# Performance work log

Hardware: AMD Instinct MI355X
Metric: run time of the kernel (lower is better)

Reference implementation:

```python
import jax, jax.numpy as jnp
import numpy as np

B, C, D, O = 262144, 256, 64, 8


def setup_inputs() -> dict:
    key = jax.random.key(0)
    k1, k2, k3, k4 = jax.random.split(key, 4)
    inputs = jax.random.normal(k1, (B, D), dtype=jnp.float32)
    cluster_centers = jax.random.normal(k2, (C, D), dtype=jnp.float32)
    # widths initialized ~ N(1.0, 0.05) as in the layer
    widths = 1.0 + 0.05 * jax.random.normal(k3, (C,), dtype=jnp.float32)
    # rule_weights ~ N(0, 0.05)
    rule_weights = 0.05 * jax.random.normal(k4, (C, O), dtype=jnp.float32)
    return {"inputs": inputs, "cluster_centers": cluster_centers,
            "widths": widths, "rule_weights": rule_weights}


def reference(inputs, cluster_centers, widths, rule_weights):
    # Squared L2 distances via ||a-c||^2 = ||a||^2 + ||c||^2 - 2 a.c
    # (avoids materializing the [B, C, D] broadcast diff tensor)
    x_sq = jnp.sum(inputs * inputs, axis=1, keepdims=True)          # [B, 1]
    c_sq = jnp.sum(cluster_centers * cluster_centers, axis=1)       # [C]
    cross = inputs @ cluster_centers.T                               # [B, C]
    dists_squared = x_sq + c_sq[None, :] - 2.0 * cross               # [B, C]
    # Gaussian membership with per-cluster widths
    memb = jnp.exp(-dists_squared / (2.0 * widths * widths))         # [B, C]
    # Normalize over clusters (sum-normalization, not softmax-of-logits)
    memb_norm = memb / jnp.sum(memb, axis=1, keepdims=True)          # [B, C]
    # Weighted rule consequents
    return memb_norm @ rule_weights                                  # [B, O]
```

## Files before the change

kernel.cpp:

```cpp
#include <hip/hip_runtime.h>


#define NB 262144
#define NC 256
#define ND 64
#define NO 8

typedef __attribute__((ext_vector_type(8))) short short8;
typedef __attribute__((ext_vector_type(16))) float floatx16;

__device__ __host__ inline unsigned short f2bf(float f) {
    unsigned u = __builtin_bit_cast(unsigned, f);
    u = u + 0x7FFFu + ((u >> 16) & 1u);
    return (unsigned short)(u >> 16);
}
__device__ inline float bf2f(unsigned short s) {
    unsigned u = ((unsigned)s) << 16;
    return __builtin_bit_cast(float, u);
}

__global__ void fuzzy_prep(const float* __restrict__ centers,
                           const float* __restrict__ widths,
                           const float* __restrict__ W,
                           unsigned short* __restrict__ ws) {
    const int lane = threadIdx.x;
    const int col = lane & 31;
    const int h = lane >> 5;

    if (blockIdx.x < 8) {
        const int t = blockIdx.x;
        const int c = 32 * t + ((col & 19) | ((col & 4) << 1) | ((col & 8) >> 1));
        const float* cr = centers + c * ND;
        float w = widths[c];
        float kk = 1.4426950408889634f / (2.0f * w * w);

        float vv[4][8];
        float part = 0.0f;
#pragma unroll
        for (int kd = 0; kd < 4; ++kd) {
            const float4* p = (const float4*)(cr + kd * 16 + h * 8);
            float4 a0 = p[0], a1 = p[1];
            vv[kd][0] = a0.x; vv[kd][1] = a0.y; vv[kd][2] = a0.z; vv[kd][3] = a0.w;
            vv[kd][4] = a1.x; vv[kd][5] = a1.y; vv[kd][6] = a1.z; vv[kd][7] = a1.w;
#pragma unroll
            for (int j = 0; j < 8; ++j) part = fmaf(vv[kd][j], vv[kd][j], part);
        }
        float csq = part + __shfl_xor(part, 32, 64);

        unsigned short* base = ws;
#pragma unroll
        for (int kd = 0; kd < 4; ++kd) {
#pragma unroll
            for (int j = 0; j < 8; ++j) {
                float a = 2.0f * kk * vv[kd][j];
                unsigned short ah = f2bf(a);
                unsigned short al = f2bf(a - bf2f(ah));
                base[((t * 9 + kd) * 64 + lane) * 8 + j] = ah;
                base[((t * 9 + 4 + kd) * 64 + lane) * 8 + j] = al;
            }
        }
        unsigned short v[8] = {0, 0, 0, 0, 0, 0, 0, 0};
        if (h == 0) {
            float Bc = csq * kk;
            float kl = kk - bf2f(f2bf(kk));
            float Bl = Bc - bf2f(f2bf(Bc));
            v[0] = f2bf(-kk);
            v[1] = f2bf(-kk);
            v[2] = f2bf(-kl);
            v[3] = f2bf(-Bc);
            v[4] = f2bf(-Bl);
        }
#pragma unroll
        for (int j = 0; j < 8; ++j)
            base[((t * 9 + 8) * 64 + lane) * 8 + j] = v[j];
    } else {
        unsigned short* wbase = ws + 8 * 9 * 64 * 8;
        const int k2base = (blockIdx.x - 8) * 4;
#pragma unroll
        for (int kq = 0; kq < 4; ++kq) {
            int k2 = k2base + kq;
#pragma unroll
            for (int j = 0; j < 8; ++j) {
                int c = k2 * 16 + h * 8 + j;
                float val = (col < NO) ? W[c * NO + col] : (col == 8 ? 1.0f : 0.0f);
                wbase[(k2 * 64 + lane) * 8 + j] = f2bf(val);
            }
        }
    }
}

__global__ __launch_bounds__(256) void fuzzy_main(const float* __restrict__ x,
                                                  const short8* __restrict__ afrag,
                                                  const short8* __restrict__ wfrag,
                                                  float* __restrict__ out) {
    const int tid = threadIdx.x;
    const int wave = tid >> 6;
    const int lane = tid & 63;
    const int col = lane & 31;
    const int h = lane >> 5;
    const int bbase = (blockIdx.x * 4 + wave) * 64;

    short8 xh[2][4], xl[2][4];
    short8 f12[2];
#pragma unroll
    for (int u = 0; u < 2; ++u) {
        const float* xrow = x + (size_t)(bbase + u * 32 + col) * ND;
        float part = 0.0f;
#pragma unroll
        for (int kd = 0; kd < 4; ++kd) {
            const float4* p = (const float4*)(xrow + kd * 16 + h * 8);
            float4 v0 = p[0], v1 = p[1];
            float v[8] = {v0.x, v0.y, v0.z, v0.w, v1.x, v1.y, v1.z, v1.w};
            short8 hi, lo;
#pragma unroll
            for (int j = 0; j < 8; ++j) {
                part = fmaf(v[j], v[j], part);
                unsigned short hb = f2bf(v[j]);
                hi[j] = (short)hb;
                lo[j] = (short)(__builtin_bit_cast(unsigned, v[j] - bf2f(hb)) >> 16);
            }
            xh[u][kd] = hi;
            xl[u][kd] = lo;
        }
        float xsq = part + __shfl_xor(part, 32, 64);
        unsigned short sh = f2bf(xsq);
        unsigned short sl = f2bf(xsq - bf2f(sh));
        short8 f;
#pragma unroll
        for (int j = 0; j < 8; ++j) f[j] = 0;
        if (h == 0) {
            f[0] = (short)sh;
            f[1] = (short)sl;
            f[2] = (short)sh;
            f[3] = (short)0x3F80;
            f[4] = (short)0x3F80;
        }
        f12[u] = f;
    }

    floatx16 acc2[2];
#pragma unroll
    for (int u = 0; u < 2; ++u)
#pragma unroll
        for (int i = 0; i < 16; ++i) acc2[u][i] = 0.0f;

    const short8* ap = afrag + lane;
    const short8* wp = wfrag + lane;

#pragma unroll 2
    for (int t = 0; t < 8; ++t) {
        short8 A0 = ap[(t * 9 + 0) * 64];
        short8 A1 = ap[(t * 9 + 1) * 64];
        short8 A2 = ap[(t * 9 + 2) * 64];
        short8 A3 = ap[(t * 9 + 3) * 64];
        short8 L0 = ap[(t * 9 + 4) * 64];
        short8 L1 = ap[(t * 9 + 5) * 64];
        short8 L2 = ap[(t * 9 + 6) * 64];
        short8 L3 = ap[(t * 9 + 7) * 64];
        short8 C12 = ap[(t * 9 + 8) * 64];
        short8 w0 = wp[(2 * t + 0) * 64];
        short8 w1 = wp[(2 * t + 1) * 64];

#pragma unroll
        for (int u = 0; u < 2; ++u) {
            floatx16 acc;
#pragma unroll
            for (int i = 0; i < 16; ++i) acc[i] = 0.0f;
            acc = __builtin_amdgcn_mfma_f32_32x32x16_bf16(A0, xh[u][0], acc, 0, 0, 0);
            acc = __builtin_amdgcn_mfma_f32_32x32x16_bf16(A1, xh[u][1], acc, 0, 0, 0);
            acc = __builtin_amdgcn_mfma_f32_32x32x16_bf16(A2, xh[u][2], acc, 0, 0, 0);
            acc = __builtin_amdgcn_mfma_f32_32x32x16_bf16(A3, xh[u][3], acc, 0, 0, 0);
            acc = __builtin_amdgcn_mfma_f32_32x32x16_bf16(L0, xh[u][0], acc, 0, 0, 0);
            acc = __builtin_amdgcn_mfma_f32_32x32x16_bf16(L1, xh[u][1], acc, 0, 0, 0);
            acc = __builtin_amdgcn_mfma_f32_32x32x16_bf16(L2, xh[u][2], acc, 0, 0, 0);
            acc = __builtin_amdgcn_mfma_f32_32x32x16_bf16(L3, xh[u][3], acc, 0, 0, 0);
            acc = __builtin_amdgcn_mfma_f32_32x32x16_bf16(A0, xl[u][0], acc, 0, 0, 0);
            acc = __builtin_amdgcn_mfma_f32_32x32x16_bf16(A1, xl[u][1], acc, 0, 0, 0);
            acc = __builtin_amdgcn_mfma_f32_32x32x16_bf16(A2, xl[u][2], acc, 0, 0, 0);
            acc = __builtin_amdgcn_mfma_f32_32x32x16_bf16(A3, xl[u][3], acc, 0, 0, 0);
            acc = __builtin_amdgcn_mfma_f32_32x32x16_bf16(C12, f12[u], acc, 0, 0, 0);

            short8 pf0, pf1;
#pragma unroll
            for (int i = 0; i < 16; ++i) {
                float p = __builtin_amdgcn_exp2f(acc[i]);
                unsigned short r = f2bf(p);
                if (i < 8) pf0[i] = (short)r;
                else       pf1[i - 8] = (short)r;
            }
            acc2[u] = __builtin_amdgcn_mfma_f32_32x32x16_bf16(w0, pf0, acc2[u], 0, 0, 0);
            acc2[u] = __builtin_amdgcn_mfma_f32_32x32x16_bf16(w1, pf1, acc2[u], 0, 0, 0);
        }
    }

#pragma unroll
    for (int u = 0; u < 2; ++u) {
        float S = acc2[u][4];
        float Sp = __shfl_xor(S, 32, 64);
        if (h) S = Sp;
        float inv = 1.0f / S;
        float4 r;
        r.x = acc2[u][0] * inv;
        r.y = acc2[u][1] * inv;
        r.z = acc2[u][2] * inv;
        r.w = acc2[u][3] * inv;
        ((float4*)(out + (size_t)(bbase + u * 32 + col) * NO))[h] = r;
    }
}

extern "C" void kernel_launch(void* const* d_in, const int* in_sizes, int n_in,
                              void* d_out, int out_size, void* d_ws, size_t ws_size,
                              hipStream_t stream) {
    const float* x       = (const float*)d_in[0];
    const float* centers = (const float*)d_in[1];
    const float* widths  = (const float*)d_in[2];
    const float* W       = (const float*)d_in[3];
    float* out = (float*)d_out;
    unsigned short* ws = (unsigned short*)d_ws;

    fuzzy_prep<<<12, 64, 0, stream>>>(centers, widths, W, ws);

    const short8* afrag = (const short8*)ws;
    const short8* wfrag = (const short8*)(ws + 8 * 9 * 64 * 8);
    fuzzy_main<<<NB / 256, 256, 0, stream>>>(x, afrag, wfrag, out);
}
```

Before: 127.2 us.

## Switch distance GEMM to single fp16 MFMA, stage fragments in LDS

Replaces the three-pass bf16 hi/lo split-precision distance product with a single fp16 pass, cutting the distance MFMAs per tile from 13 to 5. Precomputed center and weight fragments are copied into shared memory once per block instead of being reloaded from global memory. Blocks grow to 512 threads with 4 blocks per CU as the occupancy target. The exp-to-bf16 conversion becomes truncation through byte permutes instead of round-to-nearest. The trade is lower precision in the distances, which the exponent can amplify, and truncation bias in the memberships.

Measured after the change: 111.6 us. -12.3%, faster.

```diff
diff --git a/kernel.cpp b/kernel.cpp
--- a/kernel.cpp
+++ b/kernel.cpp
@@ -7,16 +7,20 @@
 #define NO 8
 
 typedef __attribute__((ext_vector_type(8))) short short8;
+typedef __attribute__((ext_vector_type(8))) _Float16 half8;
 typedef __attribute__((ext_vector_type(16))) float floatx16;
+
+#define WOFF 20480
+#define WS_SHORTS 28672
+#define WS_UINT4 3584
 
 __device__ __host__ inline unsigned short f2bf(float f) {
     unsigned u = __builtin_bit_cast(unsigned, f);
     u = u + 0x7FFFu + ((u >> 16) & 1u);
     return (unsigned short)(u >> 16);
 }
-__device__ inline float bf2f(unsigned short s) {
-    unsigned u = ((unsigned)s) << 16;
-    return __builtin_bit_cast(float, u);
+__device__ inline unsigned short f2h(float f) {
+    return __builtin_bit_cast(unsigned short, (_Float16)f);
 }
 
 __global__ void fuzzy_prep(const float* __restrict__ centers,
@@ -47,34 +51,29 @@
         }
         float csq = part + __shfl_xor(part, 32, 64);
 
-        unsigned short* base = ws;
-#pragma unroll
-        for (int kd = 0; kd < 4; ++kd) {
-#pragma unroll
-            for (int j = 0; j < 8; ++j) {
-                float a = 2.0f * kk * vv[kd][j];
-                unsigned short ah = f2bf(a);
-                unsigned short al = f2bf(a - bf2f(ah));
-                base[((t * 9 + kd) * 64 + lane) * 8 + j] = ah;
-                base[((t * 9 + 4 + kd) * 64 + lane) * 8 + j] = al;
-            }
-        }
+#pragma unroll
+        for (int kd = 0; kd < 4; ++kd)
+#pragma unroll
+            for (int j = 0; j < 8; ++j)
+                ws[((t * 5 + kd) * 64 + lane) * 8 + j] = f2h(2.0f * kk * vv[kd][j]);
+
         unsigned short v[8] = {0, 0, 0, 0, 0, 0, 0, 0};
         if (h == 0) {
+            float kh = (float)(_Float16)kk;
+            float kl = kk - kh;
             float Bc = csq * kk;
-            float kl = kk - bf2f(f2bf(kk));
-            float Bl = Bc - bf2f(f2bf(Bc));
-            v[0] = f2bf(-kk);
-            v[1] = f2bf(-kk);
-            v[2] = f2bf(-kl);
-            v[3] = f2bf(-Bc);
-            v[4] = f2bf(-Bl);
+            float Bh = (float)(_Float16)Bc;
+            float Bl = Bc - Bh;
+            v[0] = f2h(-kh);
+            v[1] = f2h(-kh);
+            v[2] = f2h(-kl);
+            v[3] = f2h(-Bh);
+            v[4] = f2h(-Bl);
         }
 #pragma unroll
         for (int j = 0; j < 8; ++j)
-            base[((t * 9 + 8) * 64 + lane) * 8 + j] = v[j];
+            ws[((t * 5 + 4) * 64 + lane) * 8 + j] = v[j];
     } else {
-        unsigned short* wbase = ws + 8 * 9 * 64 * 8;
         const int k2base = (blockIdx.x - 8) * 4;
 #pragma unroll
         for (int kq = 0; kq < 4; ++kq) {
@@ -83,25 +82,33 @@
             for (int j = 0; j < 8; ++j) {
                 int c = k2 * 16 + h * 8 + j;
                 float val = (col < NO) ? W[c * NO + col] : (col == 8 ? 1.0f : 0.0f);
-                wbase[(k2 * 64 + lane) * 8 + j] = f2bf(val);
+                ws[WOFF + (k2 * 64 + lane) * 8 + j] = f2bf(val);
             }
         }
     }
 }
 
-__global__ __launch_bounds__(256) void fuzzy_main(const float* __restrict__ x,
-                                                  const short8* __restrict__ afrag,
-                                                  const short8* __restrict__ wfrag,
-                                                  float* __restrict__ out) {
+__global__ __launch_bounds__(512, 4) void fuzzy_main(
+    const float* __restrict__ x,
+    const uint4* __restrict__ ws4,
+    float* __restrict__ out) {
+    __shared__ short lds_s[WS_SHORTS];
+
     const int tid = threadIdx.x;
     const int wave = tid >> 6;
     const int lane = tid & 63;
     const int col = lane & 31;
     const int h = lane >> 5;
-    const int bbase = (blockIdx.x * 4 + wave) * 64;
-
-    short8 xh[2][4], xl[2][4];
-    short8 f12[2];
+    const int bbase = (blockIdx.x * 8 + wave) * 64;
+
+    {
+        uint4* l4 = (uint4*)lds_s;
+#pragma unroll
+        for (int i = 0; i < 7; ++i) l4[tid + i * 512] = ws4[tid + i * 512];
+    }
+
+    half8 xh[2][4];
+    half8 f12[2];
 #pragma unroll
     for (int u = 0; u < 2; ++u) {
         const float* xrow = x + (size_t)(bbase + u * 32 + col) * ND;
@@ -111,83 +118,87 @@
             const float4* p = (const float4*)(xrow + kd * 16 + h * 8);
             float4 v0 = p[0], v1 = p[1];
             float v[8] = {v0.x, v0.y, v0.z, v0.w, v1.x, v1.y, v1.z, v1.w};
-            short8 hi, lo;
+            half8 hh;
 #pragma unroll
             for (int j = 0; j < 8; ++j) {
                 part = fmaf(v[j], v[j], part);
-                unsigned short hb = f2bf(v[j]);
-                hi[j] = (short)hb;
-                lo[j] = (short)(__builtin_bit_cast(unsigned, v[j] - bf2f(hb)) >> 16);
+                hh[j] = (_Float16)v[j];
             }
-            xh[u][kd] = hi;
-            xl[u][kd] = lo;
+            xh[u][kd] = hh;
         }
         float xsq = part + __shfl_xor(part, 32, 64);
-        unsigned short sh = f2bf(xsq);
-        unsigned short sl = f2bf(xsq - bf2f(sh));
-        short8 f;
-#pragma unroll
-        for (int j = 0; j < 8; ++j) f[j] = 0;
+        float sh = (float)(_Float16)xsq;
+        float sl = xsq - sh;
+        half8 f;
+#pragma unroll
+        for (int j = 0; j < 8; ++j) f[j] = (_Float16)0.0f;
         if (h == 0) {
-            f[0] = (short)sh;
-            f[1] = (short)sl;
-            f[2] = (short)sh;
-            f[3] = (short)0x3F80;
-            f[4] = (short)0x3F80;
+            f[0] = (_Float16)sh;
+            f[1] = (_Float16)sl;
+            f[2] = (_Float16)sh;
+            f[3] = (_Float16)1.0f;
+            f[4] = (_Float16)1.0f;
         }
         f12[u] = f;
     }
 
+    __syncthreads();
+
     floatx16 acc2[2];
 #pragma unroll
     for (int u = 0; u < 2; ++u)
 #pragma unroll
         for (int i = 0; i < 16; ++i) acc2[u][i] = 0.0f;
-
-    const short8* ap = afrag + lane;
-    const short8* wp = wfrag + lane;
 
 #pragma unroll 2
     for (int t = 0; t < 8; ++t) {
-        short8 A0 = ap[(t * 9 + 0) * 64];
-        short8 A1 = ap[(t * 9 + 1) * 64];
-        short8 A2 = ap[(t * 9 + 2) * 64];
-        short8 A3 = ap[(t * 9 + 3) * 64];
-        short8 L0 = ap[(t * 9 + 4) * 64];
-        short8 L1 = ap[(t * 9 + 5) * 64];
-        short8 L2 = ap[(t * 9 + 6) * 64];
-        short8 L3 = ap[(t * 9 + 7) * 64];
-        short8 C12 = ap[(t * 9 + 8) * 64];
-        short8 w0 = wp[(2 * t + 0) * 64];
-        short8 w1 = wp[(2 * t + 1) * 64];
+        const half8 A0 = *(const half8*)&lds_s[((t * 5 + 0) * 64 + lane) * 8];
+        const half8 A1 = *(const half8*)&lds_s[((t * 5 + 1) * 64 + lane) * 8];
+        const half8 A2 = *(const half8*)&lds_s[((t * 5 + 2) * 64 + lane) * 8];
+        const half8 A3 = *(const half8*)&lds_s[((t * 5 + 3) * 64 + lane) * 8];
+        const half8 C12 = *(const half8*)&lds_s[((t * 5 + 4) * 64 + lane) * 8];
+        const short8 w0 = *(const short8*)&lds_s[WOFF + ((2 * t + 0) * 64 + lane) * 8];
+        const short8 w1 = *(const short8*)&lds_s[WOFF + ((2 * t + 1) * 64 + lane) * 8];
 
 #pragma unroll
         for (int u = 0; u < 2; ++u) {
             floatx16 acc;
 #pragma unroll
             for (int i = 0; i < 16; ++i) acc[i] = 0.0f;
-            acc = __builtin_amdgcn_mfma_f32_32x32x16_bf16(A0, xh[u][0], acc, 0, 0, 0);
-            acc = __builtin_amdgcn_mfma_f32_32x32x16_bf16(A1, xh[u][1], acc, 0, 0, 0);
-            acc = __builtin_amdgcn_mfma_f32_32x32x16_bf16(A2, xh[u][2], acc, 0, 0, 0);
-            acc = __builtin_amdgcn_mfma_f32_32x32x16_bf16(A3, xh[u][3], acc, 0, 0, 0);
-            acc = __builtin_amdgcn_mfma_f32_32x32x16_bf16(L0, xh[u][0], acc, 0, 0, 0);
-            acc = __builtin_amdgcn_mfma_f32_32x32x16_bf16(L1, xh[u][1], acc, 0, 0, 0);
-            acc = __builtin_amdgcn_mfma_f32_32x32x16_bf16(L2, xh[u][2], acc, 0, 0, 0);
-            acc = __builtin_amdgcn_mfma_f32_32x32x16_bf16(L3, xh[u][3], acc, 0, 0, 0);
-            acc = __builtin_amdgcn_mfma_f32_32x32x16_bf16(A0, xl[u][0], acc, 0, 0, 0);
-            acc = __builtin_amdgcn_mfma_f32_32x32x16_bf16(A1, xl[u][1], acc, 0, 0, 0);
-            acc = __builtin_amdgcn_mfma_f32_32x32x16_bf16(A2, xl[u][2], acc, 0, 0, 0);
-            acc = __builtin_amdgcn_mfma_f32_32x32x16_bf16(A3, xl[u][3], acc, 0, 0, 0);
-            acc = __builtin_amdgcn_mfma_f32_32x32x16_bf16(C12, f12[u], acc, 0, 0, 0);
-
-            short8 pf0, pf1;
-#pragma unroll
-            for (int i = 0; i < 16; ++i) {
-                float p = __builtin_amdgcn_exp2f(acc[i]);
-                unsigned short r = f2bf(p);
-                if (i < 8) pf0[i] = (short)r;
-                else       pf1[i - 8] = (short)r;
-            }
+            acc = __builtin_amdgcn_mfma_f32_32x32x16_f16(A0, xh[u][0], acc, 0, 0, 0);
+            acc = __builtin_amdgcn_mfma_f32_32x32x16_f16(A1, xh[u][1], acc, 0, 0, 0);
+            acc = __builtin_amdgcn_mfma_f32_32x32x16_f16(A2, xh[u][2], acc, 0, 0, 0);
+            acc = __builtin_amdgcn_mfma_f32_32x32x16_f16(A3, xh[u][3], acc, 0, 0, 0);
+            acc = __builtin_amdgcn_mfma_f32_32x32x16_f16(C12, f12[u], acc, 0, 0, 0);
+
+            unsigned p0 = __builtin_bit_cast(unsigned, __builtin_amdgcn_exp2f(acc[0]));
+            unsigned p1 = __builtin_bit_cast(unsigned, __builtin_amdgcn_exp2f(acc[1]));
+            unsigned p2 = __builtin_bit_cast(unsigned, __builtin_amdgcn_exp2f(acc[2]));
+            unsigned p3 = __builtin_bit_cast(unsigned, __builtin_amdgcn_exp2f(acc[3]));
+            unsigned p4 = __builtin_bit_cast(unsigned, __builtin_amdgcn_exp2f(acc[4]));
+            unsigned p5 = __builtin_bit_cast(unsigned, __builtin_amdgcn_exp2f(acc[5]));
+            unsigned p6 = __builtin_bit_cast(unsigned, __builtin_amdgcn_exp2f(acc[6]));
+            unsigned p7 = __builtin_bit_cast(unsigned, __builtin_amdgcn_exp2f(acc[7]));
+            unsigned p8 = __builtin_bit_cast(unsigned, __builtin_amdgcn_exp2f(acc[8]));
+            unsigned p9 = __builtin_bit_cast(unsigned, __builtin_amdgcn_exp2f(acc[9]));
+            unsigned pa = __builtin_bit_cast(unsigned, __builtin_amdgcn_exp2f(acc[10]));
+            unsigned pb = __builtin_bit_cast(unsigned, __builtin_amdgcn_exp2f(acc[11]));
+            unsigned pc = __builtin_bit_cast(unsigned, __builtin_amdgcn_exp2f(acc[12]));
+            unsigned pd = __builtin_bit_cast(unsigned, __builtin_amdgcn_exp2f(acc[13]));
+            unsigned pe = __builtin_bit_cast(unsigned, __builtin_amdgcn_exp2f(acc[14]));
+            unsigned pf = __builtin_bit_cast(unsigned, __builtin_amdgcn_exp2f(acc[15]));
+            uint4 q0, q1;
+            q0.x = __builtin_amdgcn_perm(p1, p0, 0x07060302u);
+            q0.y = __builtin_amdgcn_perm(p3, p2, 0x07060302u);
+            q0.z = __builtin_amdgcn_perm(p5, p4, 0x07060302u);
+            q0.w = __builtin_amdgcn_perm(p7, p6, 0x07060302u);
+            q1.x = __builtin_amdgcn_perm(p9, p8, 0x07060302u);
+            q1.y = __builtin_amdgcn_perm(pb, pa, 0x07060302u);
+            q1.z = __builtin_amdgcn_perm(pd, pc, 0x07060302u);
+            q1.w = __builtin_amdgcn_perm(pf, pe, 0x07060302u);
+            short8 pf0 = __builtin_bit_cast(short8, q0);
+            short8 pf1 = __builtin_bit_cast(short8, q1);
+
             acc2[u] = __builtin_amdgcn_mfma_f32_32x32x16_bf16(w0, pf0, acc2[u], 0, 0, 0);
             acc2[u] = __builtin_amdgcn_mfma_f32_32x32x16_bf16(w1, pf1, acc2[u], 0, 0, 0);
         }
@@ -219,8 +230,5 @@
     unsigned short* ws = (unsigned short*)d_ws;
 
     fuzzy_prep<<<12, 64, 0, stream>>>(centers, widths, W, ws);
-
-    const short8* afrag = (const short8*)ws;
-    const short8* wfrag = (const short8*)(ws + 8 * 9 * 64 * 8);
-    fuzzy_main<<<NB / 256, 256, 0, stream>>>(x, afrag, wfrag, out);
-}
+    fuzzy_main<<<NB / 512, 512, 0, stream>>>(x, (const uint4*)ws, out);
+}
```
